# Optimization experiments

Measured on AMD Instinct MI355X. Metric: run time of the kernel, lower is better.

## Reference

```python
import jax, jax.numpy as jnp
import numpy as np

EMBED_DIM = 1024
NUM_HEADS = 16
HEAD_DIM = EMBED_DIM // NUM_HEADS


def setup_inputs() -> dict:
    key = jax.random.key(0)
    ks = jax.random.split(key, 8)
    B, S, D = 4, 2048, EMBED_DIM
    scale = 1.0 / np.sqrt(D)
    return {
        "values": jax.random.normal(ks[0], (B, S, D), jnp.float32),
        "keys": jax.random.normal(ks[1], (B, S, D), jnp.float32),
        "query": jax.random.normal(ks[2], (B, S, D), jnp.float32),
        "Wv": jax.random.normal(ks[3], (D, D), jnp.float32) * scale,
        "Wk": jax.random.normal(ks[4], (D, D), jnp.float32) * scale,
        "Wq": jax.random.normal(ks[5], (D, D), jnp.float32) * scale,
        "Wo": jax.random.normal(ks[6], (D, D), jnp.float32) * scale,
        "bo": jnp.zeros((D,), jnp.float32),
    }


def reference(values, keys, query, Wv, Wk, Wq, Wo, bo):
    N = query.shape[0]
    H, Dh = NUM_HEADS, HEAD_DIM
    # torch Linear: x @ W.T  (weights stored [out, in])
    v = (values @ Wv.T).reshape(N, -1, H, Dh)
    k = (keys @ Wk.T).reshape(N, -1, H, Dh)
    q = (query @ Wq.T).reshape(N, -1, H, Dh)
    # energy: [N, H, q, k]
    energy = jnp.einsum("nqhd,nkhd->nhqk", q, k)
    # NOTE: original scales by sqrt(embed_dim), not sqrt(head_dim)
    attn = jax.nn.softmax(energy / jnp.sqrt(jnp.float32(EMBED_DIM)), axis=3)
    out = jnp.einsum("nhql,nlhd->nqhd", attn, v).reshape(N, -1, H * Dh)
    return out @ Wo.T + bo
```

## Files before the change

kernel.cpp:

```cpp
#include <hip/hip_runtime.h>
#include <stdint.h>

#define S_LEN   2048
#define D_MODEL 1024
#define N_HEADS 16
#define D_HEAD  64
#define BATCH   4
#define GM      8192
#define GN      1024
#define GK      1024
#define NKT     16

typedef __attribute__((ext_vector_type(8)))  short short8;
typedef __attribute__((ext_vector_type(4)))  short short4v;
typedef __attribute__((ext_vector_type(4)))  float f32x4;
typedef __attribute__((ext_vector_type(16))) float f32x16;

__device__ __forceinline__ short f2bf(float f) {
  unsigned u = __builtin_bit_cast(unsigned, f);
  u += 0x7fffu + ((u >> 16) & 1u);
  return (short)(u >> 16);
}

__device__ __forceinline__ unsigned cvt_pk_bf16(float lo, float hi) {
  unsigned r;
  asm("v_cvt_pk_bf16_f32 %0, %1, %2" : "=v"(r) : "v"(lo), "v"(hi));
  return r;
}

__device__ __forceinline__ short8 cvtf8(const float4 f0, const float4 f1) {
  unsigned u[4] = { cvt_pk_bf16(f0.x, f0.y), cvt_pk_bf16(f0.z, f0.w),
                    cvt_pk_bf16(f1.x, f1.y), cvt_pk_bf16(f1.z, f1.w) };
  return __builtin_bit_cast(short8, *(ulonglong2*)u);
}

__device__ __forceinline__ void gload_lds16(const short* g, short* lds_base) {
  __builtin_amdgcn_global_load_lds(
      (const __attribute__((address_space(1))) void*)(const void*)g,
      (__attribute__((address_space(3))) void*)(void*)lds_base, 16, 0, 0);
}

__global__ __launch_bounds__(256)
void cast_w(const float* __restrict__ W0, const float* __restrict__ W1,
            const float* __restrict__ W2, const float* __restrict__ W3,
            short* __restrict__ O0, short* __restrict__ O1,
            short* __restrict__ O2, short* __restrict__ O3)
{
  const int y = blockIdx.y;
  const float* src = (y == 0) ? W0 : (y == 1) ? W1 : (y == 2) ? W2 : W3;
  short*       dst = (y == 0) ? O0 : (y == 1) ? O1 : (y == 2) ? O2 : O3;
  const int gid = blockIdx.x * 256 + threadIdx.x;
  const int row = gid >> 7, gr = gid & 127;
  const int og  = (gr & ~7) | ((gr & 7) ^ (row & 7));
  const float* p = src + row * 1024 + gr * 8;
  short8 v = cvtf8(*(const float4*)p, *(const float4*)(p + 4));
  *(short8*)(dst + row * 1024 + og * 8) = v;
}

__global__ __launch_bounds__(256, 2)
void gemm_qkv(const float* __restrict__ Aq, const float* __restrict__ Ak,
              const float* __restrict__ Av,
              const short* __restrict__ Bq, const short* __restrict__ Bk,
              const short* __restrict__ Bv,
              short* __restrict__ Cq, short* __restrict__ Ck,
              short* __restrict__ Cv, float qscale)
{
  __shared__ short As[3 * 8192];
  __shared__ short Bs[2 * 8192];

  const int p  = blockIdx.x + (blockIdx.y << 3) + (blockIdx.z << 9);
  const int lg = (p & 7) * 192 + (p >> 3);
  const int z  = lg >> 9;
  const int by = (lg >> 3) & 63;
  const int bx = lg & 7;

  const float* Af = (z == 0) ? Aq : (z == 1) ? Ak : Av;
  const short* Bw = (z == 0) ? Bq : (z == 1) ? Bk : Bv;

  const int t = threadIdx.x;
  const int l = t & 63, w = t >> 6;
  const int lo = l & 15, g = l >> 4;
  const int wr = (w >> 1) * 64, wc = (w & 1) * 64;

  const int srow0 = w * 8 + (l >> 3);
  const int sg = l & 7;

  f32x4 acc[4][4] = {};
  float4 aA0[4], aA1[4], aB0[4], aB1[4];

  auto issueB = [&](int kt) {
#pragma unroll
    for (int i = 0; i < 4; ++i) {
      const int row = i * 32 + srow0;
      gload_lds16(Bw + (size_t)(bx * 128 + row) * GK + kt * 64 + sg * 8,
                  (short*)((char*)Bs + (kt & 1) * 16384 + i * 4096 + w * 1024));
    }
  };
  auto loadA = [&](int kt, float4 (&s0)[4], float4 (&s1)[4]) {
#pragma unroll
    for (int i = 0; i < 4; ++i) {
      const int row = i * 32 + srow0;
      const float* pa = Af + (size_t)(by * 128 + row) * GK + kt * 64 + sg * 8;
      s0[i] = *(const float4*)pa;
      s1[i] = *(const float4*)(pa + 4);
    }
  };
  auto writeA = [&](int kt, float4 (&s0)[4], float4 (&s1)[4]) {
    const int base = (kt % 3) * 8192;
#pragma unroll
    for (int i = 0; i < 4; ++i) {
      const int row = i * 32 + srow0;
      *(short8*)(&As[base + row * 64 + ((sg ^ (row & 7)) * 8)]) = cvtf8(s0[i], s1[i]);
    }
  };
  auto compute = [&](int it) {
    const int ab = (it % 3) * 8192;
    const int bb = (it & 1) * 8192;
#pragma unroll
    for (int kh = 0; kh < 2; ++kh) {
      short8 a[4], b[4];
      const int gg = ((kh * 4 + g) ^ (lo & 7)) * 8;
#pragma unroll
      for (int mi = 0; mi < 4; ++mi)
        a[mi] = *(const short8*)(&As[ab + (wr + mi * 16 + lo) * 64 + gg]);
#pragma unroll
      for (int ni = 0; ni < 4; ++ni)
        b[ni] = *(const short8*)(&Bs[bb + (wc + ni * 16 + lo) * 64 + gg]);
#pragma unroll
      for (int mi = 0; mi < 4; ++mi)
#pragma unroll
        for (int ni = 0; ni < 4; ++ni)
          acc[mi][ni] = __builtin_amdgcn_mfma_f32_16x16x32_bf16(a[mi], b[ni], acc[mi][ni], 0, 0, 0);
    }
  };

  auto halfIter = [&](int it, float4 (&ld0)[4], float4 (&ld1)[4],
                      float4 (&wr0)[4], float4 (&wr1)[4]) {
    if (it + 1 < NKT) issueB(it + 1);
    __builtin_amdgcn_sched_barrier(0);
    if (it + 2 < NKT) loadA(it + 2, ld0, ld1);
    compute(it);
    if (it + 1 < NKT) writeA(it + 1, wr0, wr1);
    if (it + 2 < NKT)
      asm volatile("s_waitcnt vmcnt(8) lgkmcnt(0)\n\ts_barrier" ::: "memory");
    else
      asm volatile("s_waitcnt vmcnt(0) lgkmcnt(0)\n\ts_barrier" ::: "memory");
  };

  loadA(0, aA0, aA1);
  issueB(0);
  writeA(0, aA0, aA1);
  loadA(1, aB0, aB1);
  asm volatile("s_waitcnt vmcnt(8) lgkmcnt(0)\n\ts_barrier" ::: "memory");

  for (int ith = 0; ith < NKT; ith += 2) {
    halfIter(ith,     aA0, aA1, aB0, aB1);
    halfIter(ith + 1, aB0, aB1, aA0, aA1);
  }

  const int rbase = by * 128 + wr + g * 4;
  const int cbase = bx * 128 + wc + lo;

  if (z < 2) {
    short* C = (z == 0) ? Cq : Ck;
    const float scale = (z == 0) ? qscale : 1.0f;
#pragma unroll
    for (int mi = 0; mi < 4; ++mi)
#pragma unroll
      for (int ni = 0; ni < 4; ++ni)
#pragma unroll
        for (int r = 0; r < 4; ++r)
          C[(size_t)(rbase + mi * 16 + r) * GN + cbase + ni * 16] = f2bf(acc[mi][ni][r] * scale);
  } else {
#pragma unroll
    for (int mi = 0; mi < 4; ++mi)
#pragma unroll
      for (int ni = 0; ni < 4; ++ni) {
        short4v v = {f2bf(acc[mi][ni][0]), f2bf(acc[mi][ni][1]),
                     f2bf(acc[mi][ni][2]), f2bf(acc[mi][ni][3])};
        *(short4v*)(&Cv[(size_t)(cbase + ni * 16) * GM + rbase + mi * 16]) = v;
      }
  }
}

__global__ __launch_bounds__(256, 2)
void gemm_out(const short* __restrict__ Ab, const short* __restrict__ Bw,
              float* __restrict__ C, const float* __restrict__ bias)
{
  __shared__ short As[2 * 8192];
  __shared__ short Bs[2 * 8192];

  const int p  = blockIdx.x + (blockIdx.y << 3);
  const int lg = (p & 7) * 64 + (p >> 3);
  const int by = lg >> 3;
  const int bx = lg & 7;

  const int t = threadIdx.x;
  const int l = t & 63, w = t >> 6;
  const int lo = l & 15, g = l >> 4;
  const int wr = (w >> 1) * 64, wc = (w & 1) * 64;

  const int srow0 = w * 8 + (l >> 3);
  const int sg = l & 7;

  f32x4 acc[4][4] = {};

#pragma unroll
  for (int i = 0; i < 4; ++i) {
    const int row = i * 32 + srow0;
    gload_lds16(Bw + (size_t)(bx * 128 + row) * GK + sg * 8,
                (short*)((char*)Bs + i * 4096 + w * 1024));
    gload_lds16(Ab + (size_t)(by * 128 + row) * GK + sg * 8,
                (short*)((char*)As + i * 4096 + w * 1024));
  }
  __syncthreads();

  for (int it = 0; it < NKT; ++it) {
    const int cur = it & 1;
    const int nxt = cur ^ 1;

    if (it + 1 < NKT) {
      const int kn = (it + 1) * 64;
#pragma unroll
      for (int i = 0; i < 4; ++i) {
        const int row = i * 32 + srow0;
        gload_lds16(Bw + (size_t)(bx * 128 + row) * GK + kn + sg * 8,
                    (short*)((char*)Bs + nxt * 16384 + i * 4096 + w * 1024));
        gload_lds16(Ab + (size_t)(by * 128 + row) * GK + kn + sg * 8,
                    (short*)((char*)As + nxt * 16384 + i * 4096 + w * 1024));
      }
    }

#pragma unroll
    for (int kh = 0; kh < 2; ++kh) {
      short8 a[4], b[4];
      const int gg = ((kh * 4 + g) ^ (lo & 7)) * 8;
#pragma unroll
      for (int mi = 0; mi < 4; ++mi)
        a[mi] = *(const short8*)(&As[cur * 8192 + (wr + mi * 16 + lo) * 64 + gg]);
#pragma unroll
      for (int ni = 0; ni < 4; ++ni)
        b[ni] = *(const short8*)(&Bs[cur * 8192 + (wc + ni * 16 + lo) * 64 + gg]);
#pragma unroll
      for (int mi = 0; mi < 4; ++mi)
#pragma unroll
        for (int ni = 0; ni < 4; ++ni)
          acc[mi][ni] = __builtin_amdgcn_mfma_f32_16x16x32_bf16(a[mi], b[ni], acc[mi][ni], 0, 0, 0);
    }
    __syncthreads();
  }

  const int rbase = by * 128 + wr + g * 4;
  const int cbase = bx * 128 + wc + lo;
#pragma unroll
  for (int ni = 0; ni < 4; ++ni) {
    const float bs = bias[cbase + ni * 16];
#pragma unroll
    for (int mi = 0; mi < 4; ++mi)
#pragma unroll
      for (int r = 0; r < 4; ++r)
        C[(size_t)(rbase + mi * 16 + r) * GN + cbase + ni * 16] = acc[mi][ni][r] + bs;
  }
}

__global__ __launch_bounds__(512, 4)
void attn_fwd7(const short* __restrict__ Q, const short* __restrict__ Kp,
               const short* __restrict__ Vt, short* __restrict__ O)
{
  __shared__ __align__(16) char smem[49152];

  const int bid = blockIdx.x;
  const int ol = ((bid & 7) << 6) | (bid >> 3);
  const int qt = ol & 7, h = (ol >> 3) & 15, n = ol >> 7;

  const int t = threadIdx.x, w = t >> 6, l = t & 63;
  const int lq = l & 31, hi = l >> 5;

  const short* qp = Q + ((size_t)(n * S_LEN + qt * 256 + w * 32 + lq)) * D_MODEL
                      + h * D_HEAD + hi * 8;
  short8 qf[4];
#pragma unroll
  for (int kc = 0; kc < 4; ++kc) qf[kc] = *(const short8*)(qp + kc * 16);

  const int srow = t >> 3;
  const int sg0  = (t & 7) ^ (srow & 7);
  const short* kstage = Kp + ((size_t)(n * S_LEN + srow)) * D_MODEL + h * D_HEAD + sg0 * 8;
  const short* vstage = Vt + ((size_t)(h * D_HEAD + srow)) * GM + (size_t)n * S_LEN + sg0 * 8;
  const int toff = t * 16;

  auto stage = [&](int it) {
    const int kvn = it * 64;
    const int b = (it % 3) * 8192;
    gload_lds16(kstage + (size_t)kvn * D_MODEL, (short*)(smem + b + toff));
    gload_lds16(vstage + kvn,                   (short*)(smem + 24576 + b + toff));
  };

  stage(0);
  stage(1);
  asm volatile("s_waitcnt vmcnt(2)\n\ts_barrier" ::: "memory");

  f32x16 oacc[2] = {};
  float lsum = 0.f;

  const int NT = S_LEN / 64;
  for (int it = 0; it < NT; ++it) {
    const char* Kc = smem + (it % 3) * 8192;
    const char* Vc = smem + 24576 + (it % 3) * 8192;

    if (it + 2 < NT) stage(it + 2);

    f32x16 s0 = {}, s1 = {};
    __builtin_amdgcn_s_setprio(1);
#pragma unroll
    for (int kc = 0; kc < 4; ++kc) {
      const int r0 = lq, r1 = 32 + lq;
      const short8 k0 = *(const short8*)(Kc + r0 * 128 + (((kc * 2 + hi) ^ (r0 & 7)) << 4));
      const short8 k1 = *(const short8*)(Kc + r1 * 128 + (((kc * 2 + hi) ^ (r1 & 7)) << 4));
      s0 = __builtin_amdgcn_mfma_f32_32x32x16_bf16(k0, qf[kc], s0, 0, 0, 0);
      s1 = __builtin_amdgcn_mfma_f32_32x32x16_bf16(k1, qf[kc], s1, 0, 0, 0);
    }
    __builtin_amdgcn_s_setprio(0);

    float ps0 = 0.f, ps1 = 0.f, ps2 = 0.f, ps3 = 0.f;
    unsigned pk[16];
#pragma unroll
    for (int j = 0; j < 8; ++j) {
      const float p0 = __builtin_amdgcn_exp2f(s0[2 * j]);
      const float p1 = __builtin_amdgcn_exp2f(s0[2 * j + 1]);
      ps0 += p0; ps1 += p1;
      pk[j] = cvt_pk_bf16(p0, p1);
    }
#pragma unroll
    for (int j = 0; j < 8; ++j) {
      const float p0 = __builtin_amdgcn_exp2f(s1[2 * j]);
      const float p1 = __builtin_amdgcn_exp2f(s1[2 * j + 1]);
      ps2 += p0; ps3 += p1;
      pk[8 + j] = cvt_pk_bf16(p0, p1);
    }
    float psum = (ps0 + ps1) + (ps2 + ps3);
    psum += __shfl_xor(psum, 32, 64);
    lsum += psum;

    short8 pf[4];
#pragma unroll
    for (int kb = 0; kb < 2; ++kb)
#pragma unroll
      for (int ksl = 0; ksl < 2; ++ksl) {
        unsigned A0 = pk[kb * 8 + 4 * ksl];
        unsigned A1 = pk[kb * 8 + 4 * ksl + 1];
        unsigned B0 = pk[kb * 8 + 4 * ksl + 2];
        unsigned B1 = pk[kb * 8 + 4 * ksl + 3];
        asm("v_permlane32_swap_b32 %0, %1" : "+v"(A0), "+v"(B0));
        asm("v_permlane32_swap_b32 %0, %1" : "+v"(A1), "+v"(B1));
        unsigned wds[4] = {A0, A1, B0, B1};
        pf[kb * 2 + ksl] = __builtin_bit_cast(short8, *(ulonglong2*)wds);
      }

    __builtin_amdgcn_s_setprio(1);
#pragma unroll
    for (int dc = 0; dc < 2; ++dc)
#pragma unroll
      for (int ks = 0; ks < 4; ++ks) {
        const int rv = dc * 32 + lq;
        const short8 vfr = *(const short8*)(Vc + rv * 128 + (((ks * 2 + hi) ^ (rv & 7)) << 4));
        oacc[dc] = __builtin_amdgcn_mfma_f32_32x32x16_bf16(vfr, pf[ks], oacc[dc], 0, 0, 0);
      }
    __builtin_amdgcn_s_setprio(0);

    if (it + 2 < NT)
      asm volatile("s_waitcnt vmcnt(2)\n\ts_barrier" ::: "memory");
    else
      asm volatile("s_waitcnt vmcnt(0)\n\ts_barrier" ::: "memory");
  }

  short (*Os)[32][72] = (short (*)[32][72])&smem[0];
  const float inv = __builtin_amdgcn_rcpf(lsum);
#pragma unroll
  for (int dc = 0; dc < 2; ++dc)
#pragma unroll
    for (int g = 0; g < 4; ++g) {
      const int d = 32 * dc + 8 * g + 4 * hi;
      short4v v = {f2bf(oacc[dc][4 * g] * inv),     f2bf(oacc[dc][4 * g + 1] * inv),
                   f2bf(oacc[dc][4 * g + 2] * inv), f2bf(oacc[dc][4 * g + 3] * inv)};
      *(short4v*)(&Os[w][lq][d]) = v;
    }

  const int ql = l >> 1, half = l & 1;
  short* op = O + ((size_t)(n * S_LEN + qt * 256 + w * 32 + ql)) * D_MODEL + h * D_HEAD;
#pragma unroll
  for (int j = 0; j < 4; ++j) {
    const int pg = (half * 4 + j) ^ (ql & 7);
    *(short8*)(op + pg * 8) = *(const short8*)(&Os[w][ql][half * 32 + j * 8]);
  }
}

extern "C" void kernel_launch(void* const* d_in, const int* in_sizes, int n_in,
                              void* d_out, int out_size, void* d_ws, size_t ws_size,
                              hipStream_t stream) {
  const float* values = (const float*)d_in[0];
  const float* keys   = (const float*)d_in[1];
  const float* query  = (const float*)d_in[2];
  const float* Wv     = (const float*)d_in[3];
  const float* Wk     = (const float*)d_in[4];
  const float* Wq     = (const float*)d_in[5];
  const float* Wo     = (const float*)d_in[6];
  const float* bo     = (const float*)d_in[7];
  float* out = (float*)d_out;

  short* wv = (short*)d_ws;
  short* wk = wv + (size_t)1024 * 1024;
  short* wq = wk + (size_t)1024 * 1024;
  short* wo = wq + (size_t)1024 * 1024;
  short* qp = wo + (size_t)1024 * 1024;
  short* kp = qp + (size_t)GM * GN;
  short* vt = kp + (size_t)GM * GN;
  short* ao = vt + (size_t)GM * GN;

  dim3 bb(256);
  const float qscale = 0.03125f * 1.44269504089f;

  cast_w<<<dim3(512, 4), bb, 0, stream>>>(Wv, Wk, Wq, Wo, wv, wk, wq, wo);

  gemm_qkv<<<dim3(GN / 128, GM / 128, 3), bb, 0, stream>>>(
      query, keys, values, wq, wk, wv, qp, kp, vt, qscale);

  attn_fwd7<<<dim3(512), dim3(512), 0, stream>>>(qp, kp, vt, ao);

  gemm_out<<<dim3(GN / 128, GM / 128), bb, 0, stream>>>(ao, wo, out, bo);
}
```

Measured before the change: 183.3 us.

## Fuse Q/K/V projections into one persistent block looping over all three GEMMs

The QKV projection grid changes from 1536 blocks (one per tile per projection) to 512 blocks, each computing the same output tile for Q, K and V in turn. The software pipeline runs continuously across the 48 K-steps, so the prefetch for the next projection overlaps the current epilogue. This removes block launch and prologue overhead and the pipeline drain between tiles, but cuts the block count to 512, which may reduce load balance or tail behaviour on a 256-CU device.

Measured after the change: 186.5 us. Within noise of the previous version (+1.8%).

```diff
diff --git a/kernel.cpp b/kernel.cpp
--- a/kernel.cpp
+++ b/kernel.cpp
@@ -10,6 +10,7 @@
 #define GN      1024
 #define GK      1024
 #define NKT     16
+#define NGT     48
 
 typedef __attribute__((ext_vector_type(8)))  short short8;
 typedef __attribute__((ext_vector_type(4)))  short short4v;
@@ -68,14 +69,10 @@
   __shared__ short As[3 * 8192];
   __shared__ short Bs[2 * 8192];
 
-  const int p  = blockIdx.x + (blockIdx.y << 3) + (blockIdx.z << 9);
-  const int lg = (p & 7) * 192 + (p >> 3);
-  const int z  = lg >> 9;
-  const int by = (lg >> 3) & 63;
+  const int p  = blockIdx.x;
+  const int lg = (p & 7) * 64 + (p >> 3);
+  const int by = lg >> 3;
   const int bx = lg & 7;
-
-  const float* Af = (z == 0) ? Aq : (z == 1) ? Ak : Av;
-  const short* Bw = (z == 0) ? Bq : (z == 1) ? Bk : Bv;
 
   const int t = threadIdx.x;
   const int l = t & 63, w = t >> 6;
@@ -88,34 +85,45 @@
   f32x4 acc[4][4] = {};
   float4 aA0[4], aA1[4], aB0[4], aB1[4];
 
-  auto issueB = [&](int kt) {
+  auto Aof = [&](int gt) -> const float* {
+    const int z = gt >> 4; return (z == 0) ? Aq : (z == 1) ? Ak : Av;
+  };
+  auto Bof = [&](int gt) -> const short* {
+    const int z = gt >> 4; return (z == 0) ? Bq : (z == 1) ? Bk : Bv;
+  };
+
+  auto issueB = [&](int gt) {
+    const short* Bw = Bof(gt);
+    const int kk = (gt & 15) * 64;
 #pragma unroll
     for (int i = 0; i < 4; ++i) {
       const int row = i * 32 + srow0;
-      gload_lds16(Bw + (size_t)(bx * 128 + row) * GK + kt * 64 + sg * 8,
-                  (short*)((char*)Bs + (kt & 1) * 16384 + i * 4096 + w * 1024));
-    }
-  };
-  auto loadA = [&](int kt, float4 (&s0)[4], float4 (&s1)[4]) {
+      gload_lds16(Bw + (size_t)(bx * 128 + row) * GK + kk + sg * 8,
+                  (short*)((char*)Bs + (gt & 1) * 16384 + i * 4096 + w * 1024));
+    }
+  };
+  auto loadA = [&](int gt, float4 (&s0)[4], float4 (&s1)[4]) {
+    const float* Af = Aof(gt);
+    const int kk = (gt & 15) * 64;
 #pragma unroll
     for (int i = 0; i < 4; ++i) {
       const int row = i * 32 + srow0;
-      const float* pa = Af + (size_t)(by * 128 + row) * GK + kt * 64 + sg * 8;
+      const float* pa = Af + (size_t)(by * 128 + row) * GK + kk + sg * 8;
       s0[i] = *(const float4*)pa;
       s1[i] = *(const float4*)(pa + 4);
     }
   };
-  auto writeA = [&](int kt, float4 (&s0)[4], float4 (&s1)[4]) {
-    const int base = (kt % 3) * 8192;
+  auto writeA = [&](int gt, float4 (&s0)[4], float4 (&s1)[4]) {
+    const int base = (gt % 3) * 8192;
 #pragma unroll
     for (int i = 0; i < 4; ++i) {
       const int row = i * 32 + srow0;
       *(short8*)(&As[base + row * 64 + ((sg ^ (row & 7)) * 8)]) = cvtf8(s0[i], s1[i]);
     }
   };
-  auto compute = [&](int it) {
-    const int ab = (it % 3) * 8192;
-    const int bb = (it & 1) * 8192;
+  auto compute = [&](int gt) {
+    const int ab = (gt % 3) * 8192;
+    const int bb = (gt & 1) * 8192;
 #pragma unroll
     for (int kh = 0; kh < 2; ++kh) {
       short8 a[4], b[4];
@@ -134,17 +142,47 @@
     }
   };
 
-  auto halfIter = [&](int it, float4 (&ld0)[4], float4 (&ld1)[4],
+  auto halfIter = [&](int gt, float4 (&ld0)[4], float4 (&ld1)[4],
                       float4 (&wr0)[4], float4 (&wr1)[4]) {
-    if (it + 1 < NKT) issueB(it + 1);
+    if (gt + 1 < NGT) issueB(gt + 1);
     __builtin_amdgcn_sched_barrier(0);
-    if (it + 2 < NKT) loadA(it + 2, ld0, ld1);
-    compute(it);
-    if (it + 1 < NKT) writeA(it + 1, wr0, wr1);
-    if (it + 2 < NKT)
+    if (gt + 2 < NGT) loadA(gt + 2, ld0, ld1);
+    compute(gt);
+    if (gt + 1 < NGT) writeA(gt + 1, wr0, wr1);
+    if (gt + 2 < NGT)
       asm volatile("s_waitcnt vmcnt(8) lgkmcnt(0)\n\ts_barrier" ::: "memory");
     else
       asm volatile("s_waitcnt vmcnt(0) lgkmcnt(0)\n\ts_barrier" ::: "memory");
+  };
+
+  auto epilogue = [&](int z) {
+    const int rbase = by * 128 + wr + g * 4;
+    const int cbase = bx * 128 + wc + lo;
+    if (z < 2) {
+      short* C = (z == 0) ? Cq : Ck;
+      const float scale = (z == 0) ? qscale : 1.0f;
+#pragma unroll
+      for (int mi = 0; mi < 4; ++mi)
+#pragma unroll
+        for (int ni = 0; ni < 4; ++ni)
+#pragma unroll
+          for (int r = 0; r < 4; ++r)
+            C[(size_t)(rbase + mi * 16 + r) * GN + cbase + ni * 16] = f2bf(acc[mi][ni][r] * scale);
+    } else {
+#pragma unroll
+      for (int mi = 0; mi < 4; ++mi)
+#pragma unroll
+        for (int ni = 0; ni < 4; ++ni) {
+          short4v v = {f2bf(acc[mi][ni][0]), f2bf(acc[mi][ni][1]),
+                       f2bf(acc[mi][ni][2]), f2bf(acc[mi][ni][3])};
+          *(short4v*)(&Cv[(size_t)(cbase + ni * 16) * GM + rbase + mi * 16]) = v;
+        }
+    }
+#pragma unroll
+    for (int mi = 0; mi < 4; ++mi)
+#pragma unroll
+      for (int ni = 0; ni < 4; ++ni)
+        acc[mi][ni] = f32x4{0.f, 0.f, 0.f, 0.f};
   };
 
   loadA(0, aA0, aA1);
@@ -153,33 +191,14 @@
   loadA(1, aB0, aB1);
   asm volatile("s_waitcnt vmcnt(8) lgkmcnt(0)\n\ts_barrier" ::: "memory");
 
-  for (int ith = 0; ith < NKT; ith += 2) {
-    halfIter(ith,     aA0, aA1, aB0, aB1);
-    halfIter(ith + 1, aB0, aB1, aA0, aA1);
-  }
-
-  const int rbase = by * 128 + wr + g * 4;
-  const int cbase = bx * 128 + wc + lo;
-
-  if (z < 2) {
-    short* C = (z == 0) ? Cq : Ck;
-    const float scale = (z == 0) ? qscale : 1.0f;
-#pragma unroll
-    for (int mi = 0; mi < 4; ++mi)
-#pragma unroll
-      for (int ni = 0; ni < 4; ++ni)
-#pragma unroll
-        for (int r = 0; r < 4; ++r)
-          C[(size_t)(rbase + mi * 16 + r) * GN + cbase + ni * 16] = f2bf(acc[mi][ni][r] * scale);
-  } else {
-#pragma unroll
-    for (int mi = 0; mi < 4; ++mi)
-#pragma unroll
-      for (int ni = 0; ni < 4; ++ni) {
-        short4v v = {f2bf(acc[mi][ni][0]), f2bf(acc[mi][ni][1]),
-                     f2bf(acc[mi][ni][2]), f2bf(acc[mi][ni][3])};
-        *(short4v*)(&Cv[(size_t)(cbase + ni * 16) * GM + rbase + mi * 16]) = v;
-      }
+  for (int z = 0; z < 3; ++z) {
+#pragma unroll 1
+    for (int it = 0; it < NKT; it += 2) {
+      const int gt = z * 16 + it;
+      halfIter(gt,     aA0, aA1, aB0, aB1);
+      halfIter(gt + 1, aB0, aB1, aA0, aA1);
+    }
+    epilogue(z);
   }
 }
 
@@ -421,7 +440,7 @@
 
   cast_w<<<dim3(512, 4), bb, 0, stream>>>(Wv, Wk, Wq, Wo, wv, wk, wq, wo);
 
-  gemm_qkv<<<dim3(GN / 128, GM / 128, 3), bb, 0, stream>>>(
+  gemm_qkv<<<dim3(512), bb, 0, stream>>>(
       query, keys, values, wq, wk, wv, qp, kp, vt, qscale);
 
   attn_fwd7<<<dim3(512), dim3(512), 0, stream>>>(qp, kp, vt, ao);
```

## Pre-cast QKV activations to bf16 and use direct-to-LDS loads in projection GEMM

Applied to the files above, without the earlier changes.

Merges weight and activation fp32->bf16 casting into one kernel, folding the query scale into Wq. The QKV GEMM then loads bf16 A and B tiles directly into LDS with simple double buffering, dropping the register conversion and triple-buffered A staging. This removes conversion work from the GEMM's inner loop but adds an extra full pass writing and re-reading bf16 activations through memory, and the new pipeline relies on plain barriers.

Result: slower. 192.4 us (+5.0%).

```diff
diff --git a/kernel.cpp b/kernel.cpp
--- a/kernel.cpp
+++ b/kernel.cpp
@@ -41,31 +41,46 @@
 }
 
 __global__ __launch_bounds__(256)
-void cast_w(const float* __restrict__ W0, const float* __restrict__ W1,
-            const float* __restrict__ W2, const float* __restrict__ W3,
-            short* __restrict__ O0, short* __restrict__ O1,
-            short* __restrict__ O2, short* __restrict__ O3)
+void cast_all(const float* __restrict__ Iq, const float* __restrict__ Ik,
+              const float* __restrict__ Iv,
+              const float* __restrict__ W0, const float* __restrict__ W1,
+              const float* __restrict__ W2, const float* __restrict__ W3,
+              short* __restrict__ Oq, short* __restrict__ Ok,
+              short* __restrict__ Ov,
+              short* __restrict__ P0, short* __restrict__ P1,
+              short* __restrict__ P2, short* __restrict__ P3, float qscale)
 {
   const int y = blockIdx.y;
-  const float* src = (y == 0) ? W0 : (y == 1) ? W1 : (y == 2) ? W2 : W3;
-  short*       dst = (y == 0) ? O0 : (y == 1) ? O1 : (y == 2) ? O2 : O3;
+  const float* src; short* dst; float scl = 1.0f;
+  if (y == 0)      { src = Iq; dst = Oq; }
+  else if (y == 1) { src = Ik; dst = Ok; }
+  else if (y == 2) { src = Iv; dst = Ov; }
+  else {
+    if (blockIdx.x >= 512) return;
+    if (y == 3)      { src = W0; dst = P0; }
+    else if (y == 4) { src = W1; dst = P1; }
+    else if (y == 5) { src = W2; dst = P2; scl = qscale; }
+    else             { src = W3; dst = P3; }
+  }
   const int gid = blockIdx.x * 256 + threadIdx.x;
   const int row = gid >> 7, gr = gid & 127;
   const int og  = (gr & ~7) | ((gr & 7) ^ (row & 7));
-  const float* p = src + row * 1024 + gr * 8;
-  short8 v = cvtf8(*(const float4*)p, *(const float4*)(p + 4));
-  *(short8*)(dst + row * 1024 + og * 8) = v;
+  const float* p = src + (size_t)row * 1024 + gr * 8;
+  float4 f0 = *(const float4*)p, f1 = *(const float4*)(p + 4);
+  f0.x *= scl; f0.y *= scl; f0.z *= scl; f0.w *= scl;
+  f1.x *= scl; f1.y *= scl; f1.z *= scl; f1.w *= scl;
+  *(short8*)(dst + (size_t)row * 1024 + og * 8) = cvtf8(f0, f1);
 }
 
 __global__ __launch_bounds__(256, 2)
-void gemm_qkv(const float* __restrict__ Aq, const float* __restrict__ Ak,
-              const float* __restrict__ Av,
+void gemm_qkv(const short* __restrict__ Aq, const short* __restrict__ Ak,
+              const short* __restrict__ Av,
               const short* __restrict__ Bq, const short* __restrict__ Bk,
               const short* __restrict__ Bv,
               short* __restrict__ Cq, short* __restrict__ Ck,
-              short* __restrict__ Cv, float qscale)
+              short* __restrict__ Cv)
 {
-  __shared__ short As[3 * 8192];
+  __shared__ short As[2 * 8192];
   __shared__ short Bs[2 * 8192];
 
   const int p  = blockIdx.x + (blockIdx.y << 3) + (blockIdx.z << 9);
@@ -74,7 +89,7 @@
   const int by = (lg >> 3) & 63;
   const int bx = lg & 7;
 
-  const float* Af = (z == 0) ? Aq : (z == 1) ? Ak : Av;
+  const short* Ab = (z == 0) ? Aq : (z == 1) ? Ak : Av;
   const short* Bw = (z == 0) ? Bq : (z == 1) ? Bk : Bv;
 
   const int t = threadIdx.x;
@@ -86,76 +101,50 @@
   const int sg = l & 7;
 
   f32x4 acc[4][4] = {};
-  float4 aA0[4], aA1[4], aB0[4], aB1[4];
-
-  auto issueB = [&](int kt) {
-#pragma unroll
-    for (int i = 0; i < 4; ++i) {
-      const int row = i * 32 + srow0;
-      gload_lds16(Bw + (size_t)(bx * 128 + row) * GK + kt * 64 + sg * 8,
-                  (short*)((char*)Bs + (kt & 1) * 16384 + i * 4096 + w * 1024));
-    }
-  };
-  auto loadA = [&](int kt, float4 (&s0)[4], float4 (&s1)[4]) {
-#pragma unroll
-    for (int i = 0; i < 4; ++i) {
-      const int row = i * 32 + srow0;
-      const float* pa = Af + (size_t)(by * 128 + row) * GK + kt * 64 + sg * 8;
-      s0[i] = *(const float4*)pa;
-      s1[i] = *(const float4*)(pa + 4);
-    }
-  };
-  auto writeA = [&](int kt, float4 (&s0)[4], float4 (&s1)[4]) {
-    const int base = (kt % 3) * 8192;
-#pragma unroll
-    for (int i = 0; i < 4; ++i) {
-      const int row = i * 32 + srow0;
-      *(short8*)(&As[base + row * 64 + ((sg ^ (row & 7)) * 8)]) = cvtf8(s0[i], s1[i]);
-    }
-  };
-  auto compute = [&](int it) {
-    const int ab = (it % 3) * 8192;
-    const int bb = (it & 1) * 8192;
+
+#pragma unroll
+  for (int i = 0; i < 4; ++i) {
+    const int row = i * 32 + srow0;
+    gload_lds16(Bw + (size_t)(bx * 128 + row) * GK + sg * 8,
+                (short*)((char*)Bs + i * 4096 + w * 1024));
+    gload_lds16(Ab + (size_t)(by * 128 + row) * GK + sg * 8,
+                (short*)((char*)As + i * 4096 + w * 1024));
+  }
+  __syncthreads();
+
+  for (int it = 0; it < NKT; ++it) {
+    const int cur = it & 1;
+    const int nxt = cur ^ 1;
+
+    if (it + 1 < NKT) {
+      const int kn = (it + 1) * 64;
+#pragma unroll
+      for (int i = 0; i < 4; ++i) {
+        const int row = i * 32 + srow0;
+        gload_lds16(Bw + (size_t)(bx * 128 + row) * GK + kn + sg * 8,
+                    (short*)((char*)Bs + nxt * 16384 + i * 4096 + w * 1024));
+        gload_lds16(Ab + (size_t)(by * 128 + row) * GK + kn + sg * 8,
+                    (short*)((char*)As + nxt * 16384 + i * 4096 + w * 1024));
+      }
+    }
+
 #pragma unroll
     for (int kh = 0; kh < 2; ++kh) {
       short8 a[4], b[4];
       const int gg = ((kh * 4 + g) ^ (lo & 7)) * 8;
 #pragma unroll
       for (int mi = 0; mi < 4; ++mi)
-        a[mi] = *(const short8*)(&As[ab + (wr + mi * 16 + lo) * 64 + gg]);
+        a[mi] = *(const short8*)(&As[cur * 8192 + (wr + mi * 16 + lo) * 64 + gg]);
 #pragma unroll
       for (int ni = 0; ni < 4; ++ni)
-        b[ni] = *(const short8*)(&Bs[bb + (wc + ni * 16 + lo) * 64 + gg]);
+        b[ni] = *(const short8*)(&Bs[cur * 8192 + (wc + ni * 16 + lo) * 64 + gg]);
 #pragma unroll
       for (int mi = 0; mi < 4; ++mi)
 #pragma unroll
         for (int ni = 0; ni < 4; ++ni)
           acc[mi][ni] = __builtin_amdgcn_mfma_f32_16x16x32_bf16(a[mi], b[ni], acc[mi][ni], 0, 0, 0);
     }
-  };
-
-  auto halfIter = [&](int it, float4 (&ld0)[4], float4 (&ld1)[4],
-                      float4 (&wr0)[4], float4 (&wr1)[4]) {
-    if (it + 1 < NKT) issueB(it + 1);
-    __builtin_amdgcn_sched_barrier(0);
-    if (it + 2 < NKT) loadA(it + 2, ld0, ld1);
-    compute(it);
-    if (it + 1 < NKT) writeA(it + 1, wr0, wr1);
-    if (it + 2 < NKT)
-      asm volatile("s_waitcnt vmcnt(8) lgkmcnt(0)\n\ts_barrier" ::: "memory");
-    else
-      asm volatile("s_waitcnt vmcnt(0) lgkmcnt(0)\n\ts_barrier" ::: "memory");
-  };
-
-  loadA(0, aA0, aA1);
-  issueB(0);
-  writeA(0, aA0, aA1);
-  loadA(1, aB0, aB1);
-  asm volatile("s_waitcnt vmcnt(8) lgkmcnt(0)\n\ts_barrier" ::: "memory");
-
-  for (int ith = 0; ith < NKT; ith += 2) {
-    halfIter(ith,     aA0, aA1, aB0, aB1);
-    halfIter(ith + 1, aB0, aB1, aA0, aA1);
+    __syncthreads();
   }
 
   const int rbase = by * 128 + wr + g * 4;
@@ -163,14 +152,13 @@
 
   if (z < 2) {
     short* C = (z == 0) ? Cq : Ck;
-    const float scale = (z == 0) ? qscale : 1.0f;
 #pragma unroll
     for (int mi = 0; mi < 4; ++mi)
 #pragma unroll
       for (int ni = 0; ni < 4; ++ni)
 #pragma unroll
         for (int r = 0; r < 4; ++r)
-          C[(size_t)(rbase + mi * 16 + r) * GN + cbase + ni * 16] = f2bf(acc[mi][ni][r] * scale);
+          C[(size_t)(rbase + mi * 16 + r) * GN + cbase + ni * 16] = f2bf(acc[mi][ni][r]);
   } else {
 #pragma unroll
     for (int mi = 0; mi < 4; ++mi)
@@ -407,22 +395,27 @@
   const float* bo     = (const float*)d_in[7];
   float* out = (float*)d_out;
 
-  short* wv = (short*)d_ws;
-  short* wk = wv + (size_t)1024 * 1024;
-  short* wq = wk + (size_t)1024 * 1024;
-  short* wo = wq + (size_t)1024 * 1024;
-  short* qp = wo + (size_t)1024 * 1024;
-  short* kp = qp + (size_t)GM * GN;
-  short* vt = kp + (size_t)GM * GN;
-  short* ao = vt + (size_t)GM * GN;
+  short* wv  = (short*)d_ws;
+  short* wk  = wv  + (size_t)1024 * 1024;
+  short* wq  = wk  + (size_t)1024 * 1024;
+  short* wo  = wq  + (size_t)1024 * 1024;
+  short* qin = wo  + (size_t)1024 * 1024;
+  short* kin = qin + (size_t)GM * GN;
+  short* vin = kin + (size_t)GM * GN;
+  short* qp  = vin + (size_t)GM * GN;
+  short* kp  = qp  + (size_t)GM * GN;
+  short* vt  = kp  + (size_t)GM * GN;
+  short* ao  = qin;
 
   dim3 bb(256);
   const float qscale = 0.03125f * 1.44269504089f;
 
-  cast_w<<<dim3(512, 4), bb, 0, stream>>>(Wv, Wk, Wq, Wo, wv, wk, wq, wo);
-
-  gemm_qkv<<<dim3(GN / 128, GM / 128, 3), bb, 0, stream>>>(
-      query, keys, values, wq, wk, wv, qp, kp, vt, qscale);
+  cast_all<<<dim3(4096, 7), bb, 0, stream>>>(
+      query, keys, values, Wv, Wk, Wq, Wo,
+      qin, kin, vin, wv, wk, wq, wo, qscale);
+
+  gemm_qkv<<<dim3(8, 64, 3), bb, 0, stream>>>(
+      qin, kin, vin, wq, wk, wv, qp, kp, vt);
 
   attn_fwd7<<<dim3(512), dim3(512), 0, stream>>>(qp, kp, vt, ao);
 
```

## Use 512-thread blocks with 8 waves in QKV projection GEMM

Applied to the files above, without the earlier changes.

The QKV GEMM block grows from 256 to 512 threads. The 128x128 tile is split over 8 waves, each computing 64x32, so per-thread accumulators and A-staging registers are halved. The fp32 A loads and B async copies are spread over more threads, with the vmcnt waits adjusted to match. This aims to raise wave occupancy and hide latency, but it halves per-wave MFMA reuse and adds more LDS reads per MFMA.

Measured after the change: 175.6 us. 1.04x faster.

```diff
diff --git a/kernel.cpp b/kernel.cpp
--- a/kernel.cpp
+++ b/kernel.cpp
@@ -57,7 +57,7 @@
   *(short8*)(dst + row * 1024 + og * 8) = v;
 }
 
-__global__ __launch_bounds__(256, 2)
+__global__ __launch_bounds__(512, 4)
 void gemm_qkv(const float* __restrict__ Aq, const float* __restrict__ Ak,
               const float* __restrict__ Av,
               const short* __restrict__ Bq, const short* __restrict__ Bk,
@@ -80,37 +80,39 @@
   const int t = threadIdx.x;
   const int l = t & 63, w = t >> 6;
   const int lo = l & 15, g = l >> 4;
-  const int wr = (w >> 1) * 64, wc = (w & 1) * 64;
-
-  const int srow0 = w * 8 + (l >> 3);
-  const int sg = l & 7;
-
-  f32x4 acc[4][4] = {};
-  float4 aA0[4], aA1[4], aB0[4], aB1[4];
+  const int wr = (w >> 2) * 64;
+  const int wc = (w & 3) * 32;
+
+  f32x4 acc[4][2] = {};
+  float4 aA[4], aB[4];
 
   auto issueB = [&](int kt) {
 #pragma unroll
-    for (int i = 0; i < 4; ++i) {
-      const int row = i * 32 + srow0;
+    for (int i = 0; i < 2; ++i) {
+      const int gid = i * 512 + t;
+      const int row = gid >> 3;
+      const int sg  = gid & 7;
       gload_lds16(Bw + (size_t)(bx * 128 + row) * GK + kt * 64 + sg * 8,
-                  (short*)((char*)Bs + (kt & 1) * 16384 + i * 4096 + w * 1024));
-    }
-  };
-  auto loadA = [&](int kt, float4 (&s0)[4], float4 (&s1)[4]) {
-#pragma unroll
-    for (int i = 0; i < 4; ++i) {
-      const int row = i * 32 + srow0;
-      const float* pa = Af + (size_t)(by * 128 + row) * GK + kt * 64 + sg * 8;
-      s0[i] = *(const float4*)pa;
-      s1[i] = *(const float4*)(pa + 4);
-    }
-  };
-  auto writeA = [&](int kt, float4 (&s0)[4], float4 (&s1)[4]) {
+                  (short*)((char*)Bs + (kt & 1) * 16384 + gid * 16));
+    }
+  };
+  auto loadA = [&](int kt, float4 (&s)[4]) {
+#pragma unroll
+    for (int i = 0; i < 2; ++i) {
+      const int u = i * 512 + t;
+      const int row = u >> 3, c8 = u & 7;
+      const float* pa = Af + (size_t)(by * 128 + row) * GK + kt * 64 + c8 * 8;
+      s[2 * i]     = *(const float4*)pa;
+      s[2 * i + 1] = *(const float4*)(pa + 4);
+    }
+  };
+  auto writeA = [&](int kt, float4 (&s)[4]) {
     const int base = (kt % 3) * 8192;
 #pragma unroll
-    for (int i = 0; i < 4; ++i) {
-      const int row = i * 32 + srow0;
-      *(short8*)(&As[base + row * 64 + ((sg ^ (row & 7)) * 8)]) = cvtf8(s0[i], s1[i]);
+    for (int i = 0; i < 2; ++i) {
+      const int u = i * 512 + t;
+      const int row = u >> 3, c8 = u & 7;
+      *(short8*)(&As[base + row * 64 + ((c8 ^ (row & 7)) * 8)]) = cvtf8(s[2 * i], s[2 * i + 1]);
     }
   };
   auto compute = [&](int it) {
@@ -118,44 +120,43 @@
     const int bb = (it & 1) * 8192;
 #pragma unroll
     for (int kh = 0; kh < 2; ++kh) {
-      short8 a[4], b[4];
+      short8 a[4], b[2];
       const int gg = ((kh * 4 + g) ^ (lo & 7)) * 8;
 #pragma unroll
       for (int mi = 0; mi < 4; ++mi)
         a[mi] = *(const short8*)(&As[ab + (wr + mi * 16 + lo) * 64 + gg]);
 #pragma unroll
-      for (int ni = 0; ni < 4; ++ni)
+      for (int ni = 0; ni < 2; ++ni)
         b[ni] = *(const short8*)(&Bs[bb + (wc + ni * 16 + lo) * 64 + gg]);
 #pragma unroll
       for (int mi = 0; mi < 4; ++mi)
 #pragma unroll
-        for (int ni = 0; ni < 4; ++ni)
+        for (int ni = 0; ni < 2; ++ni)
           acc[mi][ni] = __builtin_amdgcn_mfma_f32_16x16x32_bf16(a[mi], b[ni], acc[mi][ni], 0, 0, 0);
     }
   };
 
-  auto halfIter = [&](int it, float4 (&ld0)[4], float4 (&ld1)[4],
-                      float4 (&wr0)[4], float4 (&wr1)[4]) {
+  auto halfIter = [&](int it, float4 (&ld)[4], float4 (&wrs)[4]) {
     if (it + 1 < NKT) issueB(it + 1);
     __builtin_amdgcn_sched_barrier(0);
-    if (it + 2 < NKT) loadA(it + 2, ld0, ld1);
+    if (it + 2 < NKT) loadA(it + 2, ld);
     compute(it);
-    if (it + 1 < NKT) writeA(it + 1, wr0, wr1);
+    if (it + 1 < NKT) writeA(it + 1, wrs);
     if (it + 2 < NKT)
-      asm volatile("s_waitcnt vmcnt(8) lgkmcnt(0)\n\ts_barrier" ::: "memory");
+      asm volatile("s_waitcnt vmcnt(4) lgkmcnt(0)\n\ts_barrier" ::: "memory");
     else
       asm volatile("s_waitcnt vmcnt(0) lgkmcnt(0)\n\ts_barrier" ::: "memory");
   };
 
-  loadA(0, aA0, aA1);
+  loadA(0, aA);
   issueB(0);
-  writeA(0, aA0, aA1);
-  loadA(1, aB0, aB1);
-  asm volatile("s_waitcnt vmcnt(8) lgkmcnt(0)\n\ts_barrier" ::: "memory");
+  writeA(0, aA);
+  loadA(1, aB);
+  asm volatile("s_waitcnt vmcnt(4) lgkmcnt(0)\n\ts_barrier" ::: "memory");
 
   for (int ith = 0; ith < NKT; ith += 2) {
-    halfIter(ith,     aA0, aA1, aB0, aB1);
-    halfIter(ith + 1, aB0, aB1, aA0, aA1);
+    halfIter(ith,     aA, aB);
+    halfIter(ith + 1, aB, aA);
   }
 
   const int rbase = by * 128 + wr + g * 4;
@@ -167,7 +168,7 @@
 #pragma unroll
     for (int mi = 0; mi < 4; ++mi)
 #pragma unroll
-      for (int ni = 0; ni < 4; ++ni)
+      for (int ni = 0; ni < 2; ++ni)
 #pragma unroll
         for (int r = 0; r < 4; ++r)
           C[(size_t)(rbase + mi * 16 + r) * GN + cbase + ni * 16] = f2bf(acc[mi][ni][r] * scale);
@@ -175,7 +176,7 @@
 #pragma unroll
     for (int mi = 0; mi < 4; ++mi)
 #pragma unroll
-      for (int ni = 0; ni < 4; ++ni) {
+      for (int ni = 0; ni < 2; ++ni) {
         short4v v = {f2bf(acc[mi][ni][0]), f2bf(acc[mi][ni][1]),
                      f2bf(acc[mi][ni][2]), f2bf(acc[mi][ni][3])};
         *(short4v*)(&Cv[(size_t)(cbase + ni * 16) * GM + rbase + mi * 16]) = v;
@@ -421,7 +422,7 @@
 
   cast_w<<<dim3(512, 4), bb, 0, stream>>>(Wv, Wk, Wq, Wo, wv, wk, wq, wo);
 
-  gemm_qkv<<<dim3(GN / 128, GM / 128, 3), bb, 0, stream>>>(
+  gemm_qkv<<<dim3(GN / 128, GM / 128, 3), dim3(512), 0, stream>>>(
       query, keys, values, wq, wk, wv, qp, kp, vt, qscale);
 
   attn_fwd7<<<dim3(512), dim3(512), 0, stream>>>(qp, kp, vt, ao);
```
